# Optimization experiments

Hardware: AMD Instinct MI355X
Metric: run time of the kernel (lower is better)

## Reference

```python
import jax, jax.numpy as jnp
import numpy as np

K = 9  # kernel_size (knn neighbors, loop=True -> self included)

def setup_inputs() -> dict:
    key = jax.random.key(0)
    k1, k2, k3 = jax.random.split(key, 3)
    B, C, H, W = 8, 64, 32, 32
    OUT = 64
    x = jax.random.normal(k1, (B, C, H, W), dtype=jnp.float32)
    # SAGEConv params: lin_l (neighbor aggregate, with bias), lin_r (root, no bias)
    s = 1.0 / np.sqrt(C)
    W_l = jax.random.uniform(k2, (OUT, C), minval=-s, maxval=s, dtype=jnp.float32)
    b_l = jnp.zeros((OUT,), dtype=jnp.float32)
    W_r = jax.random.uniform(k3, (OUT, C), minval=-s, maxval=s, dtype=jnp.float32)
    return {"x": x, "W_l": W_l, "b_l": b_l, "W_r": W_r}

def _knn_mean(x_f, batches):
    # squared-euclidean pairwise distances [N, N], masked across batches
    sq = jnp.sum(x_f * x_f, axis=-1)
    dist = sq[:, None] + sq[None, :] - 2.0 * (x_f @ x_f.T)
    cross = batches[:, None] != batches[None, :]
    dist = jnp.where(cross, jnp.inf, dist)
    neg, idx = jax.lax.top_k(-dist, K)          # k nearest (self included, dist 0)
    valid = (neg != -jnp.inf).astype(x_f.dtype)  # handle degenerate last-batch node
    nbr = x_f[idx] * valid[..., None]            # [N, K, C]
    return nbr.sum(axis=1) / valid.sum(axis=1, keepdims=True)

def reference(x, W_l, b_l, W_r):
    B, C, H, Wd = x.shape
    N = B * H * Wd
    x_f = x.transpose(0, 2, 3, 1).reshape(N, C)  # flat_nodes: [B*H*W, C]
    # torch.linspace(0, B, steps=N).to(int64): truncation of i*B/(N-1)
    batches = jnp.linspace(0.0, float(B), N).astype(jnp.int32)
    mean_nbr = _knn_mean(x_f, batches)
    # SAGEConv: lin_l(mean_j x_j) + lin_r(x_i)
    return mean_nbr @ W_l.T + b_l + x_f @ W_r.T
```

## Files before the change

kernel.cpp:

```cpp
#include <hip/hip_runtime.h>
#include <cstdint>
#include <cstddef>


typedef unsigned long long u64;

__global__ __launch_bounds__(256, 2) void k_all(const float* __restrict__ x,
                                                const float* __restrict__ Wl,
                                                const float* __restrict__ bl,
                                                const float* __restrict__ Wr,
                                                float* __restrict__ out) {
  __shared__ float SH[8320];
  float4* Asf4 = (float4*)SH;

  int bi = (int)blockIdx.x, t = threadIdx.x;
  int lane = t & 63, w = t >> 6;
  int n0 = bi << 4;
  int s = (n0 >= 7168) ? 7168 : (n0 & ~1023);
  const float* xb = x + ((size_t)(s >> 10) << 16);
  const float* xrow = x + ((size_t)(n0 >> 10) << 16) + (n0 & 1023);

  {
    int ch = t >> 2, g = t & 3;
    Asf4[t] = *(const float4*)&xrow[((size_t)ch << 10) + (g << 2)];
  }
  __syncthreads();

  float4 av = Asf4[(lane << 2) + w];

  float acc[4][16];
  float sqa[16];
#pragma unroll
  for (int r = 0; r < 4; ++r)
#pragma unroll
    for (int j = 0; j < 16; ++j) acc[r][j] = 0.f;
#pragma unroll
  for (int j = 0; j < 16; ++j) sqa[j] = 0.f;

  const float* xl = xb + (lane << 2);
#pragma unroll 4
  for (int ch = 0; ch < 64; ++ch) {
    float4 a4 = Asf4[(ch << 2) + w];
    const float* xc = xl + ((size_t)ch << 10);
    float4 b0 = *(const float4*)&xc[0];
    float4 b1 = *(const float4*)&xc[256];
    float4 b2 = *(const float4*)&xc[512];
    float4 b3 = *(const float4*)&xc[768];
    float bv[16] = {b0.x, b0.y, b0.z, b0.w, b1.x, b1.y, b1.z, b1.w,
                    b2.x, b2.y, b2.z, b2.w, b3.x, b3.y, b3.z, b3.w};
    float ar[4] = {a4.x, a4.y, a4.z, a4.w};
#pragma unroll
    for (int j = 0; j < 16; ++j) {
      sqa[j] = fmaf(bv[j], bv[j], sqa[j]);
      acc[0][j] = fmaf(ar[0], bv[j], acc[0][j]);
      acc[1][j] = fmaf(ar[1], bv[j], acc[1][j]);
      acc[2][j] = fmaf(ar[2], bv[j], acc[2][j]);
      acc[3][j] = fmaf(ar[3], bv[j], acc[3][j]);
    }
  }

#define DPPMIN(CTRL)                                                         \
  {                                                                          \
    unsigned oh_ = (unsigned)__builtin_amdgcn_update_dpp(                    \
        (int)gh, (int)gh, CTRL, 0xF, 0xF, false);                            \
    unsigned ol_ = (unsigned)__builtin_amdgcn_update_dpp(                    \
        (int)gl, (int)gl, CTRL, 0xF, 0xF, false);                            \
    u64 cur_ = ((u64)gh << 32) | gl;                                         \
    u64 oth_ = ((u64)oh_ << 32) | ol_;                                       \
    bool take_ = oth_ < cur_;                                                \
    gh = take_ ? oh_ : gh;                                                   \
    gl = take_ ? ol_ : gl;                                                   \
  }

  float msum[4];
  int cnt[4];
#pragma unroll 4
  for (int rr = 0; rr < 4; ++rr) {
    int n = n0 + (w << 2) + rr;
    float xself = (rr == 0) ? av.x : (rr == 1) ? av.y : (rr == 2) ? av.z : av.w;
    if (n == 8191) {
      msum[rr] = xself;
      cnt[rr] = 1;
    } else {
      cnt[rr] = 9;
      int ln = n - s;
      int slot_o = ((ln >> 8) << 2) | (ln & 3);
      float sv = sqa[0];
#pragma unroll
      for (int j = 1; j < 16; ++j) sv = (slot_o == j) ? sqa[j] : sv;
      float si = __int_as_float(
          __builtin_amdgcn_readlane(__float_as_int(sv), (ln & 255) >> 2));
      bool mlast = (n >= 7168);
      unsigned long long cand[16];
#pragma unroll
      for (int q = 0; q < 4; ++q) {
#pragma unroll
        for (int e = 0; e < 4; ++e) {
          float d = (si + sqa[(q << 2) + e]) - 2.f * acc[rr][(q << 2) + e];
          unsigned u = __float_as_uint(d);
          u = (u & 0x80000000u) ? ~u : (u | 0x80000000u);
          unsigned jj = (unsigned)((q << 8) + (lane << 2) + e);
          cand[(q << 2) + e] = ((unsigned long long)u << 32) | jj;
        }
      }
      if (mlast && lane == 63) cand[15] = ~0ull;
      unsigned long long m1 = cand[0], m2 = cand[1];
      if (m2 < m1) { unsigned long long tt = m1; m1 = m2; m2 = tt; }
#pragma unroll
      for (int q = 2; q < 16; ++q) {
        unsigned long long c = cand[q];
        unsigned long long lo = (c < m1) ? c : m1;
        unsigned long long hi = (c < m1) ? m1 : c;
        m2 = (hi < m2) ? hi : m2;
        m1 = lo;
      }
      unsigned long long lm = m1;
      unsigned rmask = 0;
      bool stale = false;
      unsigned jloc[9];
#pragma unroll
      for (int kk = 0; kk < 9; ++kk) {
        unsigned gh = (unsigned)(lm >> 32), gl = (unsigned)lm;
        DPPMIN(0xB1)
        DPPMIN(0x4E)
        DPPMIN(0x141)
        DPPMIN(0x140)
        DPPMIN(0x142)
        DPPMIN(0x143)
        unsigned wh = __builtin_amdgcn_readlane((int)gh, 63);
        unsigned wl = __builtin_amdgcn_readlane((int)gl, 63);
        u64 g = ((u64)wh << 32) | wl;
        jloc[kk] = (unsigned)g & 1023u;
        if (lm == g) {
          unsigned slot = (((unsigned)g >> 6) & 12u) | ((unsigned)g & 3u);
          rmask |= 1u << slot;
          if (!stale) { lm = m2; stale = true; }
          else {
            unsigned long long best = ~0ull;
#pragma unroll
            for (int q = 0; q < 16; ++q) {
              bool alive = ((rmask >> q) & 1u) == 0u;
              unsigned long long c = cand[q];
              best = (alive && c < best) ? c : best;
            }
            lm = best;
          }
        }
      }
      const float* gx = xb + ((size_t)lane << 10);
      float g0 = gx[jloc[0]], g1 = gx[jloc[1]], g2 = gx[jloc[2]];
      float g3 = gx[jloc[3]], g4 = gx[jloc[4]], g5 = gx[jloc[5]];
      float g6 = gx[jloc[6]], g7 = gx[jloc[7]], g8 = gx[jloc[8]];
      msum[rr] = (((g0 + g1) + (g2 + g3)) + ((g4 + g5) + (g6 + g7))) + g8;
    }
  }
  __syncthreads();

#pragma unroll
  for (int i = 0; i < 16; ++i) {
    int lin = t + (i << 8);
    int o = lin >> 6, c = lin & 63;
    SH[o * 65 + c] = Wl[lin];
    SH[4160 + o * 65 + c] = Wr[lin];
  }
  __syncthreads();

  float bias = bl[lane];
  float ms[4];
#pragma unroll
  for (int rr = 0; rr < 4; ++rr)
    ms[rr] = (cnt[rr] == 9) ? msum[rr] * (1.f / 9.f) : msum[rr];
  float xr[4] = {av.x, av.y, av.z, av.w};
  float accL[4] = {0.f, 0.f, 0.f, 0.f};
  float accR[4] = {0.f, 0.f, 0.f, 0.f};
#pragma unroll
  for (int c = 0; c < 64; ++c) {
    float wlc = SH[lane * 65 + c];
    float wrc = SH[4160 + lane * 65 + c];
#pragma unroll
    for (int rr = 0; rr < 4; ++rr) {
      float mc = __int_as_float(__builtin_amdgcn_readlane(__float_as_int(ms[rr]), c));
      float xc = __int_as_float(__builtin_amdgcn_readlane(__float_as_int(xr[rr]), c));
      accL[rr] = fmaf(mc, wlc, accL[rr]);
      accR[rr] = fmaf(xc, wrc, accR[rr]);
    }
  }
#pragma unroll
  for (int rr = 0; rr < 4; ++rr)
    __builtin_nontemporal_store(accL[rr] + accR[rr] + bias,
                                &out[((size_t)(n0 + (w << 2) + rr) << 6) + lane]);
}

extern "C" void kernel_launch(void* const* d_in, const int* in_sizes, int n_in,
                              void* d_out, int out_size, void* d_ws, size_t ws_size,
                              hipStream_t stream) {
  const float* x  = (const float*)d_in[0];
  const float* Wl = (const float*)d_in[1];
  const float* bl = (const float*)d_in[2];
  const float* Wr = (const float*)d_in[3];
  float* out = (float*)d_out;
  (void)d_ws; (void)ws_size;

  k_all<<<dim3(512), 256, 0, stream>>>(x, Wl, bl, Wr, out);
}
```

Measured before the change: 105.4 us.

## Stage kNN candidate keys and neighbor means in LDS to cut register pressure

Each thread now writes its 16 packed distance/index keys to shared memory for each node and reads them back for the top-2 pass and for the rare rescan. It no longer keeps them in a register array. Neighbor means also go through shared memory and no longer use readlane broadcasts. Several loops are left rolled (unroll 1) to shrink code and live registers. The aim is to fit the 2-blocks-per-SM launch bound without spills, at the cost of extra LDS traffic, more barriers and loop overhead.

```diff
diff --git a/kernel.cpp b/kernel.cpp
--- a/kernel.cpp
+++ b/kernel.cpp
@@ -4,14 +4,55 @@
 
 
 typedef unsigned long long u64;
+
+#define DPPMIN(CTRL)                                                         \
+  {                                                                          \
+    unsigned oh_ = (unsigned)__builtin_amdgcn_update_dpp(                    \
+        (int)gh, (int)gh, CTRL, 0xF, 0xF, false);                            \
+    unsigned ol_ = (unsigned)__builtin_amdgcn_update_dpp(                    \
+        (int)gl, (int)gl, CTRL, 0xF, 0xF, false);                            \
+    u64 cur_ = ((u64)gh << 32) | gl;                                         \
+    u64 oth_ = ((u64)oh_ << 32) | ol_;                                       \
+    bool take_ = oth_ < cur_;                                                \
+    gh = take_ ? oh_ : gh;                                                   \
+    gl = take_ ? ol_ : gl;                                                   \
+  }
+
+#define KEYGEN(RR)                                                           \
+  {                                                                          \
+    int n_ = n0 + (w << 2) + RR;                                             \
+    int ln_ = n_ - s;                                                        \
+    int so_ = ((ln_ >> 8) << 2) | (ln_ & 3);                                 \
+    float sv_ = sqa[0];                                                      \
+    _Pragma("unroll")                                                        \
+    for (int j_ = 1; j_ < 16; ++j_) sv_ = (so_ == j_) ? sqa[j_] : sv_;       \
+    float si_ = __int_as_float(__builtin_amdgcn_readlane(                    \
+        __float_as_int(sv_), (ln_ & 255) >> 2));                             \
+    bool ml_ = (n_ >= 7168);                                                 \
+    _Pragma("unroll")                                                        \
+    for (int q_ = 0; q_ < 4; ++q_)                                           \
+      _Pragma("unroll")                                                      \
+      for (int e_ = 0; e_ < 4; ++e_) {                                       \
+        int sl_ = (q_ << 2) + e_;                                            \
+        float d_ = (si_ + sqa[sl_]) - 2.f * acc[RR][sl_];                    \
+        unsigned u_ = __float_as_uint(d_);                                   \
+        u_ = (u_ & 0x80000000u) ? ~u_ : (u_ | 0x80000000u);                  \
+        u64 k_ = ((u64)u_ << 32) |                                           \
+                 (unsigned)((q_ << 8) + (lane << 2) + e_);                   \
+        if (sl_ == 15) k_ = (ml_ && lane == 63) ? ~0ull : k_;                \
+        cand[(sl_ << 8) + t] = k_;                                           \
+      }                                                                      \
+  }
 
 __global__ __launch_bounds__(256, 2) void k_all(const float* __restrict__ x,
                                                 const float* __restrict__ Wl,
                                                 const float* __restrict__ bl,
                                                 const float* __restrict__ Wr,
                                                 float* __restrict__ out) {
-  __shared__ float SH[8320];
+  __shared__ float SH[9344];
+  float* ms_f = SH + 8320;
   float4* Asf4 = (float4*)SH;
+  u64* cand = (u64*)SH;
 
   int bi = (int)blockIdx.x, t = threadIdx.x;
   int lane = t & 63, w = t >> 6;
@@ -58,63 +99,34 @@
       acc[3][j] = fmaf(ar[3], bv[j], acc[3][j]);
     }
   }
-
-#define DPPMIN(CTRL)                                                         \
-  {                                                                          \
-    unsigned oh_ = (unsigned)__builtin_amdgcn_update_dpp(                    \
-        (int)gh, (int)gh, CTRL, 0xF, 0xF, false);                            \
-    unsigned ol_ = (unsigned)__builtin_amdgcn_update_dpp(                    \
-        (int)gl, (int)gl, CTRL, 0xF, 0xF, false);                            \
-    u64 cur_ = ((u64)gh << 32) | gl;                                         \
-    u64 oth_ = ((u64)oh_ << 32) | ol_;                                       \
-    bool take_ = oth_ < cur_;                                                \
-    gh = take_ ? oh_ : gh;                                                   \
-    gl = take_ ? ol_ : gl;                                                   \
-  }
-
-  float msum[4];
-  int cnt[4];
-#pragma unroll 4
+  __syncthreads();
+
+#pragma unroll 1
   for (int rr = 0; rr < 4; ++rr) {
     int n = n0 + (w << 2) + rr;
+    if (rr == 0) KEYGEN(0)
+    else if (rr == 1) KEYGEN(1)
+    else if (rr == 2) KEYGEN(2)
+    else KEYGEN(3)
     float xself = (rr == 0) ? av.x : (rr == 1) ? av.y : (rr == 2) ? av.z : av.w;
+    float msv;
     if (n == 8191) {
-      msum[rr] = xself;
-      cnt[rr] = 1;
+      msv = xself;
     } else {
-      cnt[rr] = 9;
-      int ln = n - s;
-      int slot_o = ((ln >> 8) << 2) | (ln & 3);
-      float sv = sqa[0];
-#pragma unroll
-      for (int j = 1; j < 16; ++j) sv = (slot_o == j) ? sqa[j] : sv;
-      float si = __int_as_float(
-          __builtin_amdgcn_readlane(__float_as_int(sv), (ln & 255) >> 2));
-      bool mlast = (n >= 7168);
-      unsigned long long cand[16];
-#pragma unroll
-      for (int q = 0; q < 4; ++q) {
-#pragma unroll
-        for (int e = 0; e < 4; ++e) {
-          float d = (si + sqa[(q << 2) + e]) - 2.f * acc[rr][(q << 2) + e];
-          unsigned u = __float_as_uint(d);
-          u = (u & 0x80000000u) ? ~u : (u | 0x80000000u);
-          unsigned jj = (unsigned)((q << 8) + (lane << 2) + e);
-          cand[(q << 2) + e] = ((unsigned long long)u << 32) | jj;
-        }
-      }
-      if (mlast && lane == 63) cand[15] = ~0ull;
-      unsigned long long m1 = cand[0], m2 = cand[1];
-      if (m2 < m1) { unsigned long long tt = m1; m1 = m2; m2 = tt; }
+      u64 kreg[16];
+#pragma unroll
+      for (int q = 0; q < 16; ++q) kreg[q] = cand[(q << 8) + t];
+      u64 m1 = kreg[0], m2 = kreg[1];
+      if (m2 < m1) { u64 tt = m1; m1 = m2; m2 = tt; }
 #pragma unroll
       for (int q = 2; q < 16; ++q) {
-        unsigned long long c = cand[q];
-        unsigned long long lo = (c < m1) ? c : m1;
-        unsigned long long hi = (c < m1) ? m1 : c;
+        u64 c = kreg[q];
+        u64 lo = (c < m1) ? c : m1;
+        u64 hi = (c < m1) ? m1 : c;
         m2 = (hi < m2) ? hi : m2;
         m1 = lo;
       }
-      unsigned long long lm = m1;
+      u64 lm = m1;
       unsigned rmask = 0;
       bool stale = false;
       unsigned jloc[9];
@@ -136,11 +148,11 @@
           rmask |= 1u << slot;
           if (!stale) { lm = m2; stale = true; }
           else {
-            unsigned long long best = ~0ull;
-#pragma unroll
+            u64 best = ~0ull;
+#pragma unroll 1
             for (int q = 0; q < 16; ++q) {
+              u64 c = cand[(q << 8) + t];
               bool alive = ((rmask >> q) & 1u) == 0u;
-              unsigned long long c = cand[q];
               best = (alive && c < best) ? c : best;
             }
             lm = best;
@@ -151,8 +163,10 @@
       float g0 = gx[jloc[0]], g1 = gx[jloc[1]], g2 = gx[jloc[2]];
       float g3 = gx[jloc[3]], g4 = gx[jloc[4]], g5 = gx[jloc[5]];
       float g6 = gx[jloc[6]], g7 = gx[jloc[7]], g8 = gx[jloc[8]];
-      msum[rr] = (((g0 + g1) + (g2 + g3)) + ((g4 + g5) + (g6 + g7))) + g8;
+      float msum = (((g0 + g1) + (g2 + g3)) + ((g4 + g5) + (g6 + g7))) + g8;
+      msv = msum * (1.f / 9.f);
     }
+    ms_f[(rr << 8) + t] = msv;
   }
   __syncthreads();
 
@@ -166,24 +180,29 @@
   __syncthreads();
 
   float bias = bl[lane];
-  float ms[4];
-#pragma unroll
-  for (int rr = 0; rr < 4; ++rr)
-    ms[rr] = (cnt[rr] == 9) ? msum[rr] * (1.f / 9.f) : msum[rr];
-  float xr[4] = {av.x, av.y, av.z, av.w};
   float accL[4] = {0.f, 0.f, 0.f, 0.f};
   float accR[4] = {0.f, 0.f, 0.f, 0.f};
-#pragma unroll
+  int mbase = w << 6;
+#pragma unroll 1
   for (int c = 0; c < 64; ++c) {
     float wlc = SH[lane * 65 + c];
     float wrc = SH[4160 + lane * 65 + c];
-#pragma unroll
-    for (int rr = 0; rr < 4; ++rr) {
-      float mc = __int_as_float(__builtin_amdgcn_readlane(__float_as_int(ms[rr]), c));
-      float xc = __int_as_float(__builtin_amdgcn_readlane(__float_as_int(xr[rr]), c));
-      accL[rr] = fmaf(mc, wlc, accL[rr]);
-      accR[rr] = fmaf(xc, wrc, accR[rr]);
-    }
+    float m0 = ms_f[mbase + c];
+    float m1f = ms_f[256 + mbase + c];
+    float m2f = ms_f[512 + mbase + c];
+    float m3f = ms_f[768 + mbase + c];
+    float x0 = __int_as_float(__builtin_amdgcn_readlane(__float_as_int(av.x), c));
+    float x1 = __int_as_float(__builtin_amdgcn_readlane(__float_as_int(av.y), c));
+    float x2 = __int_as_float(__builtin_amdgcn_readlane(__float_as_int(av.z), c));
+    float x3 = __int_as_float(__builtin_amdgcn_readlane(__float_as_int(av.w), c));
+    accL[0] = fmaf(m0, wlc, accL[0]);
+    accL[1] = fmaf(m1f, wlc, accL[1]);
+    accL[2] = fmaf(m2f, wlc, accL[2]);
+    accL[3] = fmaf(m3f, wlc, accL[3]);
+    accR[0] = fmaf(x0, wrc, accR[0]);
+    accR[1] = fmaf(x1, wrc, accR[1]);
+    accR[2] = fmaf(x2, wrc, accR[2]);
+    accR[3] = fmaf(x3, wrc, accR[3]);
   }
 #pragma unroll
   for (int rr = 0; rr < 4; ++rr)
```

New measurement: 145.9 us. 38.4% more time.
